# Performance work log

Hardware: AMD Instinct MI355X
Metric: run time of the kernel (lower is better)

Reference implementation:

```python
import jax, jax.numpy as jnp
import numpy as np


def setup_inputs() -> dict:
    key = jax.random.key(0)
    k1, k2 = jax.random.split(key)
    query = jax.random.normal(k1, (1, 1024), dtype=jnp.float32)
    keys = jax.random.normal(k2, (32768, 1024), dtype=jnp.float32)
    return {"query": query, "keys": keys}


def reference(query, keys):
    # query: [1, H] -> squeeze to [H]; keys: [S, H]
    q = jnp.squeeze(query)                       # [H]
    dots = keys @ q                              # [S]
    q_norm = jnp.linalg.norm(q)                  # scalar
    k_norms = jnp.linalg.norm(keys, axis=-1)     # [S]
    cos_scores = dots / (q_norm * k_norms)       # [S] cosine similarity per key
    context = jnp.sum(cos_scores[:, None] * keys, axis=0)  # [H]
    return context[None, :]                      # [1, H]
```

## Files before the change

### kernel.cpp

```cpp
#include <hip/hip_runtime.h>


constexpr int H   = 1024;
constexpr int TPB = 256;
constexpr int WPB = TPB / 64;
constexpr int NBLOCKS = 512;
constexpr int R2_CHUNKS = 16;


template <bool USE_WS>
__global__ __launch_bounds__(TPB, 2)
void cosctx_main(const float* __restrict__ q,
                 const float* __restrict__ keys,
                 int S,
                 float* __restrict__ out,
                 float* __restrict__ ws)
{
    const int lane  = threadIdx.x & 63;
    const int wave  = threadIdx.x >> 6;
    const int gwave = blockIdx.x * WPB + wave;
    const int nwaves = gridDim.x * WPB;

    const float4* q4 = reinterpret_cast<const float4*>(q);
    const float4* k4 = reinterpret_cast<const float4*>(keys);

    float4 qv[4];
#pragma unroll
    for (int j = 0; j < 4; ++j) qv[j] = q4[j * 64 + lane];

    float qsq = 0.f;
#pragma unroll
    for (int j = 0; j < 4; ++j)
        qsq += qv[j].x * qv[j].x + qv[j].y * qv[j].y +
               qv[j].z * qv[j].z + qv[j].w * qv[j].w;
#pragma unroll
    for (int off = 32; off > 0; off >>= 1) qsq += __shfl_down(qsq, off, 64);
    const float inv_qn = rsqrtf(__shfl(qsq, 0, 64));

    float4 acc[4];
#pragma unroll
    for (int j = 0; j < 4; ++j) acc[j] = make_float4(0.f, 0.f, 0.f, 0.f);

    int row = gwave;
    float4 kv[4];
    if (row < S) {
        const float4* kr = k4 + (size_t)row * (H / 4);
#pragma unroll
        for (int j = 0; j < 4; ++j) kv[j] = kr[j * 64 + lane];
    }
    while (row < S) {
        const int nrow = row + nwaves;
        float4 kn[4];
        if (nrow < S) {
            const float4* kr = k4 + (size_t)nrow * (H / 4);
#pragma unroll
            for (int j = 0; j < 4; ++j) kn[j] = kr[j * 64 + lane];
        }

        float dot = 0.f, ksq = 0.f;
#pragma unroll
        for (int j = 0; j < 4; ++j) {
            dot += kv[j].x * qv[j].x + kv[j].y * qv[j].y +
                   kv[j].z * qv[j].z + kv[j].w * qv[j].w;
            ksq += kv[j].x * kv[j].x + kv[j].y * kv[j].y +
                   kv[j].z * kv[j].z + kv[j].w * kv[j].w;
        }
#pragma unroll
        for (int off = 32; off > 0; off >>= 1) {
            dot += __shfl_down(dot, off, 64);
            ksq += __shfl_down(ksq, off, 64);
        }
        const float score = __shfl(dot, 0, 64) * inv_qn *
                            rsqrtf(__shfl(ksq, 0, 64));

#pragma unroll
        for (int j = 0; j < 4; ++j) {
            acc[j].x += score * kv[j].x;
            acc[j].y += score * kv[j].y;
            acc[j].z += score * kv[j].z;
            acc[j].w += score * kv[j].w;
        }
#pragma unroll
        for (int j = 0; j < 4; ++j) kv[j] = kn[j];
        row = nrow;
    }

    __shared__ float sacc[WPB][H];
    float4* sa4 = reinterpret_cast<float4*>(sacc[wave]);
#pragma unroll
    for (int j = 0; j < 4; ++j) sa4[j * 64 + lane] = acc[j];
    __syncthreads();

    float4 v = make_float4(0.f, 0.f, 0.f, 0.f);
#pragma unroll
    for (int w = 0; w < WPB; ++w) {
        float4 u = reinterpret_cast<const float4*>(sacc[w])[threadIdx.x];
        v.x += u.x; v.y += u.y; v.z += u.z; v.w += u.w;
    }

    if (USE_WS) {
        reinterpret_cast<float4*>(ws)[(size_t)blockIdx.x * (H / 4) + threadIdx.x] = v;
    } else {
        const int c = threadIdx.x * 4;
        atomicAdd(out + c + 0, v.x);
        atomicAdd(out + c + 1, v.y);
        atomicAdd(out + c + 2, v.z);
        atomicAdd(out + c + 3, v.w);
    }
}

__global__ __launch_bounds__(256)
void cosctx_reduce(const float* __restrict__ ws, float* __restrict__ out)
{
    const int g  = blockIdx.x & 3;
    const int ch = blockIdx.x >> 2;
    const int c  = g * 256 + threadIdx.x;
    const int bpc = NBLOCKS / R2_CHUNKS;
    const int b0 = ch * bpc;
    float s = 0.f;
#pragma unroll 4
    for (int b = b0; b < b0 + bpc; ++b)
        s += ws[(size_t)b * H + c];
    atomicAdd(out + c, s);
}

extern "C" void kernel_launch(void* const* d_in, const int* in_sizes, int n_in,
                              void* d_out, int out_size, void* d_ws, size_t ws_size,
                              hipStream_t stream)
{
    const float* q    = (const float*)d_in[0];
    const float* keys = (const float*)d_in[1];
    float* out        = (float*)d_out;
    const int S = in_sizes[1] / H;

    hipMemsetAsync(out, 0, H * sizeof(float), stream);

    const size_t ws_need = (size_t)NBLOCKS * H * sizeof(float);
    if (ws_size >= ws_need) {
        cosctx_main<true><<<NBLOCKS, TPB, 0, stream>>>(q, keys, S, out, (float*)d_ws);
        cosctx_reduce<<<4 * R2_CHUNKS, 256, 0, stream>>>((const float*)d_ws, out);
    } else {
        cosctx_main<false><<<NBLOCKS, TPB, 0, stream>>>(q, keys, S, out, nullptr);
    }
}
```

Measured before the change: 194.6 us.

## Fuse cross-block reduction into main kernel via atomics and double grid size

```diff
diff --git a/kernel.cpp b/kernel.cpp
--- a/kernel.cpp
+++ b/kernel.cpp
@@ -4,17 +4,13 @@
 constexpr int H   = 1024;
 constexpr int TPB = 256;
 constexpr int WPB = TPB / 64;
-constexpr int NBLOCKS = 512;
-constexpr int R2_CHUNKS = 16;
+constexpr int NBLOCKS = 1024;
 
-
-template <bool USE_WS>
-__global__ __launch_bounds__(TPB, 2)
-void cosctx_main(const float* __restrict__ q,
-                 const float* __restrict__ keys,
-                 int S,
-                 float* __restrict__ out,
-                 float* __restrict__ ws)
+__global__ __launch_bounds__(TPB, 4)
+void cosctx_fused(const float* __restrict__ q,
+                  const float* __restrict__ keys,
+                  int S,
+                  float* __restrict__ out)
 {
     const int lane  = threadIdx.x & 63;
     const int wave  = threadIdx.x >> 6;
@@ -98,30 +94,11 @@
         v.x += u.x; v.y += u.y; v.z += u.z; v.w += u.w;
     }
 
-    if (USE_WS) {
-        reinterpret_cast<float4*>(ws)[(size_t)blockIdx.x * (H / 4) + threadIdx.x] = v;
-    } else {
-        const int c = threadIdx.x * 4;
-        atomicAdd(out + c + 0, v.x);
-        atomicAdd(out + c + 1, v.y);
-        atomicAdd(out + c + 2, v.z);
-        atomicAdd(out + c + 3, v.w);
-    }
-}
-
-__global__ __launch_bounds__(256)
-void cosctx_reduce(const float* __restrict__ ws, float* __restrict__ out)
-{
-    const int g  = blockIdx.x & 3;
-    const int ch = blockIdx.x >> 2;
-    const int c  = g * 256 + threadIdx.x;
-    const int bpc = NBLOCKS / R2_CHUNKS;
-    const int b0 = ch * bpc;
-    float s = 0.f;
-#pragma unroll 4
-    for (int b = b0; b < b0 + bpc; ++b)
-        s += ws[(size_t)b * H + c];
-    atomicAdd(out + c, s);
+    const int c = threadIdx.x * 4;
+    atomicAdd(out + c + 0, v.x);
+    atomicAdd(out + c + 1, v.y);
+    atomicAdd(out + c + 2, v.z);
+    atomicAdd(out + c + 3, v.w);
 }
 
 extern "C" void kernel_launch(void* const* d_in, const int* in_sizes, int n_in,
@@ -134,12 +111,5 @@
     const int S = in_sizes[1] / H;
 
     hipMemsetAsync(out, 0, H * sizeof(float), stream);
-
-    const size_t ws_need = (size_t)NBLOCKS * H * sizeof(float);
-    if (ws_size >= ws_need) {
-        cosctx_main<true><<<NBLOCKS, TPB, 0, stream>>>(q, keys, S, out, (float*)d_ws);
-        cosctx_reduce<<<4 * R2_CHUNKS, 256, 0, stream>>>((const float*)d_ws, out);
-    } else {
-        cosctx_main<false><<<NBLOCKS, TPB, 0, stream>>>(q, keys, S, out, nullptr);
-    }
+    cosctx_fused<<<NBLOCKS, TPB, 0, stream>>>(q, keys, S, out);
 }
```

Result: slower. 277.0 us (+42.4%).
